# Optimization experiments

Measured on AMD Instinct MI355X. Metric: run time of the kernel, lower is better.

## Reference

```python
import jax, jax.numpy as jnp
import numpy as np

W_DIM = 72  # positional_encoding(3 coords, 12 freqs) -> 3*12*2
_F1 = np.array([1.0, 3.0, 3.0, 1.0], dtype=np.float32)
_F2 = np.outer(_F1, _F1); _F2 = _F2 / _F2.sum()  # normalized StyleGAN resample filter


def upsample2x(x):
    """Antialiased 2x upsample: zero-insertion + 4-tap [1,3,3,1] FIR, gain=4 (upfirdn2d)."""
    C = x.shape[1]
    k = jnp.tile(jnp.asarray(_F2 * 4.0, x.dtype)[None, None], (C, 1, 1, 1))  # [C,1,4,4]
    return jax.lax.conv_general_dilated(
        x, k, (1, 1), ((2, 2), (2, 2)), lhs_dilation=(2, 2),
        feature_group_count=C, dimension_numbers=('NCHW', 'OIHW', 'NCHW'))


def affine(w_vec, aw, ab):
    # FullyConnectedLayer: runtime weight gain 1/sqrt(w_dim), bias init 1
    return (w_vec @ aw.T) / np.sqrt(W_DIM) + ab


def mod_conv(x, weight, styles, demodulate=True, padding=1):
    """StyleGAN2 modulated conv2d (batch=1). weight [Co,Ci,k,k], styles [Ci]."""
    w = weight * styles[None, :, None, None]
    if demodulate:
        d = jax.lax.rsqrt(jnp.sum(w * w, axis=(1, 2, 3)) + 1e-8)
        w = w * d[:, None, None, None]
    return jax.lax.conv_general_dilated(
        x, w, (1, 1), ((padding, padding), (padding, padding)),
        dimension_numbers=('NCHW', 'OIHW', 'NCHW'))


def syn_layer(x, w_vec, aw, ab, cw, cb, up):
    s = affine(w_vec, aw, ab)
    if up:
        x = upsample2x(x)
    x = mod_conv(x, cw, s, True, 1)
    # bias_act: lrelu, gain sqrt(2), conv_clamp 256 (noise_strength init 0 -> no noise)
    x = jax.nn.leaky_relu(x + cb[None, :, None, None], 0.2) * np.sqrt(2.0)
    return jnp.clip(x, -256.0, 256.0)


def to_rgb(x, w_vec, aw, ab, cw, cb):
    s = affine(w_vec, aw, ab) / np.sqrt(cw.shape[1])  # ToRGB weight_gain 1/sqrt(Cin)
    y = mod_conv(x, cw, s, False, 0)
    return jnp.clip(y + cb[None, :, None, None], -256.0, 256.0)


def reference(rays, rgbs, conv_w, conv_b, bn_gamma, bn_beta, bn_mean, bn_var,
              a0_w, a0_b, w0, b0, a1_w, a1_b, w1, b1, t0_aw, t0_ab, t0_w, t0_b,
              a2_w, a2_b, w2, b2, a3_w, a3_b, w3, b3, t1_aw, t1_ab, t1_w, t1_b):
    # style vector from positional encoding of ray origin
    p = rays[0, :3, 0, 0]
    fb = 2.0 ** jnp.arange(12, dtype=rays.dtype)
    pts = (p[:, None] * fb[None, :]).reshape(-1)  # (36,)
    w_vec = jnp.concatenate([jnp.sin(pts), jnp.cos(pts)])  # (72,)
    # mapping: 1x1 conv + relu + BatchNorm2d (eval-mode)
    feat = jnp.einsum('oi,bihw->bohw', conv_w[:, :, 0, 0], rgbs) + conv_b[None, :, None, None]
    feat = jax.nn.relu(feat)
    inv = jax.lax.rsqrt(bn_var + 1e-5)
    feat = (feat - bn_mean[None, :, None, None]) * (inv * bn_gamma)[None, :, None, None] + bn_beta[None, :, None, None]
    rgb = feat[:, :3]
    # block0: 32ch@128 -> 256ch@256, skip-architecture ToRGB
    x = syn_layer(feat, w_vec, a0_w, a0_b, w0, b0, True)
    x = syn_layer(x, w_vec, a1_w, a1_b, w1, b1, False)
    img = upsample2x(rgb) + to_rgb(x, w_vec, t0_aw, t0_ab, t0_w, t0_b)
    # block1: 256ch@256 -> 128ch@512
    x = syn_layer(x, w_vec, a2_w, a2_b, w2, b2, True)
    x = syn_layer(x, w_vec, a3_w, a3_b, w3, b3, False)
    img = upsample2x(img) + to_rgb(x, w_vec, t1_aw, t1_ab, t1_w, t1_b)
    return img  # [1,3,512,512]


def setup_inputs() -> dict:
    key = jax.random.key(0)
    ks = jax.random.split(key, 16)
    rn = lambda k, s: jax.random.normal(k, s, dtype=jnp.float32)
    z = lambda s: jnp.zeros(s, jnp.float32)
    o = lambda s: jnp.ones(s, jnp.float32)
    inp = {}
    inp['rays'] = rn(ks[0], (1, 6, 128, 128))
    inp['rgbs'] = jax.random.uniform(ks[1], (1, 3, 128, 128), dtype=jnp.float32)
    inp['conv_w'] = rn(ks[2], (32, 3, 1, 1)); inp['conv_b'] = z((32,))
    inp['bn_gamma'] = o((32,)); inp['bn_beta'] = z((32,))
    inp['bn_mean'] = z((32,)); inp['bn_var'] = o((32,))
    inp['a0_w'] = rn(ks[3], (32, 72)); inp['a0_b'] = o((32,))
    inp['w0'] = rn(ks[4], (256, 32, 3, 3)); inp['b0'] = z((256,))
    inp['a1_w'] = rn(ks[5], (256, 72)); inp['a1_b'] = o((256,))
    inp['w1'] = rn(ks[6], (256, 256, 3, 3)); inp['b1'] = z((256,))
    inp['t0_aw'] = rn(ks[7], (256, 72)); inp['t0_ab'] = o((256,))
    inp['t0_w'] = rn(ks[8], (3, 256, 1, 1)); inp['t0_b'] = z((3,))
    inp['a2_w'] = rn(ks[9], (256, 72)); inp['a2_b'] = o((256,))
    inp['w2'] = rn(ks[10], (128, 256, 3, 3)); inp['b2'] = z((128,))
    inp['a3_w'] = rn(ks[11], (128, 72)); inp['a3_b'] = o((128,))
    inp['w3'] = rn(ks[12], (128, 128, 3, 3)); inp['b3'] = z((128,))
    inp['t1_aw'] = rn(ks[13], (128, 72)); inp['t1_ab'] = o((128,))
    inp['t1_w'] = rn(ks[14], (3, 128, 1, 1)); inp['t1_b'] = z((3,))
    return inp
```

## Files before the change

### kernel.cpp

```cpp
#include <hip/hip_runtime.h>
#include <cstddef>

typedef __attribute__((ext_vector_type(8))) short short8;
typedef __attribute__((ext_vector_type(4))) float f32x4;
typedef __attribute__((address_space(3))) void lds_void;
typedef const __attribute__((address_space(1))) void glob_void;

static const size_t OFF_S0    = 0;
static const size_t OFF_S1    = 64;
static const size_t OFF_S2    = 320;
static const size_t OFF_S3    = 576;
static const size_t OFF_MT0   = 704;
static const size_t OFF_MT1   = 1472;
static const size_t OFF_ZERO  = 1856;
static const size_t OFF_RGBF  = 2048;
static const size_t OFF_IMG0  = 51200;
static const size_t OFF_RGBP  = 247808;
static const size_t OFF_WQ0   = 1900544;
static const size_t OFF_WQ1   = 1937408;
static const size_t OFF_WQ2   = 2232320;
static const size_t OFF_WQ3   = 2379776;
static const size_t OFF_FEAT  = 2453504;
static const size_t OFF_UFEAT = 2715648;
static const size_t OFF_X1    = 4194304;
static const size_t OFF_X2    = 4194304;
static const size_t OFF_U     = 20971520;
static const size_t OFF_X0    = 20971520;

__device__ __forceinline__ unsigned short f2bf(float f) {
  unsigned int u = __float_as_uint(f);
  return (unsigned short)((u + 0x7FFFu + ((u >> 16) & 1u)) >> 16);
}
__device__ __forceinline__ float b2f(short h) {
  return __uint_as_float(((unsigned int)(unsigned short)h) << 16);
}

__global__ void __launch_bounds__(256) prep_kernel(
    const float* __restrict__ rays,
    const float* __restrict__ a0w, const float* __restrict__ a0b,
    const float* __restrict__ a1w, const float* __restrict__ a1b,
    const float* __restrict__ t0aw, const float* __restrict__ t0ab,
    const float* __restrict__ a2w, const float* __restrict__ a2b,
    const float* __restrict__ a3w, const float* __restrict__ a3b,
    const float* __restrict__ t1aw, const float* __restrict__ t1ab,
    const float* __restrict__ t0w, const float* __restrict__ t1w,
    float* __restrict__ ws)
{
  __shared__ float wv[72];
  __shared__ float st0l[256];
  __shared__ float st1l[128];
  const int tid = threadIdx.x;
  if (tid < 128) ws[OFF_ZERO + tid] = 0.f;
  if (tid < 36) {
    int i = tid / 12, j = tid % 12;
    float v = rays[i * 16384] * (float)(1 << j);
    wv[tid]      = sinf(v);
    wv[36 + tid] = cosf(v);
  }
  __syncthreads();
  const float inv72 = 0.11785113019775793f;

  if (tid < 32) {
    float d = 0.f;
    for (int k = 0; k < 72; ++k) d += wv[k] * a0w[tid * 72 + k];
    ws[OFF_S0 + tid] = fmaf(d, inv72, a0b[tid]);
  }
  {
    float d = 0.f;
    for (int k = 0; k < 72; ++k) d += wv[k] * a1w[tid * 72 + k];
    ws[OFF_S1 + tid] = fmaf(d, inv72, a1b[tid]);
  }
  {
    float d = 0.f;
    for (int k = 0; k < 72; ++k) d += wv[k] * t0aw[tid * 72 + k];
    st0l[tid] = fmaf(d, inv72, t0ab[tid]) * 0.0625f;
  }
  {
    float d = 0.f;
    for (int k = 0; k < 72; ++k) d += wv[k] * a2w[tid * 72 + k];
    ws[OFF_S2 + tid] = fmaf(d, inv72, a2b[tid]);
  }
  if (tid < 128) {
    float d = 0.f;
    for (int k = 0; k < 72; ++k) d += wv[k] * a3w[tid * 72 + k];
    ws[OFF_S3 + tid] = fmaf(d, inv72, a3b[tid]);
  }
  if (tid < 128) {
    float d = 0.f;
    for (int k = 0; k < 72; ++k) d += wv[k] * t1aw[tid * 72 + k];
    st1l[tid] = fmaf(d, inv72, t1ab[tid]) * 0.08838834764831845f;
  }
  __syncthreads();
  for (int i = tid; i < 768; i += 256) ws[OFF_MT0 + i] = t0w[i] * st0l[i & 255];
  for (int i = tid; i < 384; i += 256) ws[OFF_MT1 + i] = t1w[i] * st1l[i & 127];
}

__global__ void __launch_bounds__(256) modw_kernel(
    const float* __restrict__ w, const float* __restrict__ s,
    unsigned short* __restrict__ wq, int Ci, int Co)
{
  const int co = blockIdx.x;
  const int n = Ci * 9;
  float local = 0.f;
  for (int i = threadIdx.x; i < n; i += 256) {
    float v = w[co * n + i] * s[i / 9];
    local += v * v;
  }
#pragma unroll
  for (int off = 32; off >= 1; off >>= 1) local += __shfl_xor(local, off);
  __shared__ float red[4];
  if ((threadIdx.x & 63) == 0) red[threadIdx.x >> 6] = local;
  __syncthreads();
  const float d = rsqrtf(red[0] + red[1] + red[2] + red[3] + 1e-8f);
  for (int i = threadIdx.x; i < n; i += 256) {
    int ci = i / 9, t = i - ci * 9;
    wq[(((size_t)(ci >> 5) * 9 + t) * Co + co) * 32 + (ci & 31)] =
        f2bf(w[co * n + i] * s[ci] * d);
  }
}

__global__ void __launch_bounds__(256) feat_kernel(
    const float* __restrict__ rgbs, const float* __restrict__ cw, const float* __restrict__ cb,
    const float* __restrict__ gam, const float* __restrict__ bet,
    const float* __restrict__ mean, const float* __restrict__ var,
    unsigned short* __restrict__ feat, float* __restrict__ rgbf)
{
  const int p = blockIdx.x * 256 + threadIdx.x;
  const float r = rgbs[p], g = rgbs[16384 + p], b = rgbs[32768 + p];
  unsigned int pk[16];
#pragma unroll
  for (int co = 0; co < 32; ++co) {
    float v = cw[co * 3] * r + cw[co * 3 + 1] * g + cw[co * 3 + 2] * b + cb[co];
    v = fmaxf(v, 0.f);
    float inv = rsqrtf(var[co] + 1e-5f);
    v = (v - mean[co]) * (inv * gam[co]) + bet[co];
    if (co < 3) rgbf[co * 16384 + p] = v;
    unsigned int h = f2bf(v);
    if ((co & 1) == 0) pk[co >> 1] = h;
    else               pk[co >> 1] |= h << 16;
  }
  uint4* dst = reinterpret_cast<uint4*>(feat + (size_t)p * 32);
#pragma unroll
  for (int q = 0; q < 4; ++q)
    dst[q] = make_uint4(pk[q * 4], pk[q * 4 + 1], pk[q * 4 + 2], pk[q * 4 + 3]);
}

__global__ void __launch_bounds__(256) up2x_nhwc_kernel(
    const unsigned short* __restrict__ in, unsigned short* __restrict__ out,
    int H, int W, int c8s , int w2s )
{
  const int cid = blockIdx.x * 256 + threadIdx.x;
  const int k = cid & ((1 << c8s) - 1);
  const int pix = cid >> c8s;
  const int ey = pix >> w2s;
  const int ex = pix & ((1 << w2s) - 1);
  const int C = 8 << c8s;
  int ry0; float ay0, ay1;
  if (ey & 1) { ry0 = ey >> 1;       ay0 = 0.75f; ay1 = 0.25f; }
  else        { ry0 = (ey >> 1) - 1; ay0 = 0.25f; ay1 = 0.75f; }
  int cx0; float bx0, bx1;
  if (ex & 1) { cx0 = ex >> 1;       bx0 = 0.75f; bx1 = 0.25f; }
  else        { cx0 = (ex >> 1) - 1; bx0 = 0.25f; bx1 = 0.75f; }
  const short8 z = {0, 0, 0, 0, 0, 0, 0, 0};
  short8 v00 = z, v01 = z, v10 = z, v11 = z;
  const bool yo0 = (ry0 >= 0), yo1 = (ry0 + 1 < H);
  const bool xo0 = (cx0 >= 0), xo1 = (cx0 + 1 < W);
  if (yo0 && xo0) v00 = *reinterpret_cast<const short8*>(in + ((size_t)(ry0 * W + cx0) * C + k * 8));
  if (yo0 && xo1) v01 = *reinterpret_cast<const short8*>(in + ((size_t)(ry0 * W + cx0 + 1) * C + k * 8));
  if (yo1 && xo0) v10 = *reinterpret_cast<const short8*>(in + ((size_t)((ry0 + 1) * W + cx0) * C + k * 8));
  if (yo1 && xo1) v11 = *reinterpret_cast<const short8*>(in + ((size_t)((ry0 + 1) * W + cx0 + 1) * C + k * 8));
  unsigned int o[4];
#pragma unroll
  for (int j = 0; j < 8; ++j) {
    float f = ay0 * (bx0 * b2f(v00[j]) + bx1 * b2f(v01[j]))
            + ay1 * (bx0 * b2f(v10[j]) + bx1 * b2f(v11[j]));
    unsigned int h = f2bf(f);
    if ((j & 1) == 0) o[j >> 1] = h;
    else              o[j >> 1] |= h << 16;
  }
  *reinterpret_cast<uint4*>(out + (size_t)pix * C + k * 8) = make_uint4(o[0], o[1], o[2], o[3]);
}

template <bool FUSE_RGB>
__global__ void __launch_bounds__(512) conv3x3_mfma(
    const unsigned short* __restrict__ in,
    const unsigned short* __restrict__ wq,
    const float* __restrict__ bias,
    unsigned short* __restrict__ out,
    const float* __restrict__ rgbw,
    float* __restrict__ rgbp,
    const unsigned short* __restrict__ zpage,
    int H, int W, int Ci, int Co)
{
  const int tid  = threadIdx.x;
  const int lane = tid & 63;
  const int wv   = tid >> 6;
  const int wr   = wv & 3;
  const int wg   = wv >> 2;
  const int lo   = lane & 15, hi = lane >> 4;
  const int tpr  = W >> 4;
  const int T_y  = (blockIdx.x / tpr) << 4;
  const int T_x  = (blockIdx.x % tpr) << 4;
  const int cog  = (blockIdx.y * 2 + wg) << 6;

  __shared__ short8 xs[2][1296];
  __shared__ float  rw[FUSE_RGB ? 384 : 4];

  if (FUSE_RGB) {
    for (int i = tid; i < 3 * Co; i += 512) rw[i] = rgbw[i];
  }

  f32x4 acc[4][4];
#pragma unroll
  for (int a = 0; a < 4; ++a)
#pragma unroll
    for (int b = 0; b < 4; ++b) acc[a][b] = (f32x4){0.f, 0.f, 0.f, 0.f};

  const unsigned short* gsrc[3];
#pragma unroll
  for (int j = 0; j < 3; ++j) {
    const int s = j * 512 + tid;
    const int pix = s >> 2, kslot = s & 3;
    const int rr = pix / 18, cc = pix - rr * 18;
    const int gy = T_y - 1 + rr, gx = T_x - 1 + cc;
    const int k = kslot ^ ((cc >> 1) & 3);
    const bool inb = (s < 1296) && gy >= 0 && gy < H && gx >= 0 && gx < W;
    gsrc[j] = inb ? (in + ((size_t)(gy * W + gx) * Ci + (k << 3))) : zpage;
  }

#define STAGE(c, buf)                                                              \
  {                                                                                \
    const int cb_ = (c) << 5;                                                      \
    _Pragma("unroll")                                                              \
    for (int j = 0; j < 2; ++j)                                                    \
      __builtin_amdgcn_global_load_lds((glob_void*)(gsrc[j] + cb_),                \
                                       (lds_void*)&xs[buf][j * 512 + tid], 16, 0, 0); \
    if (tid < 272)                                                                 \
      __builtin_amdgcn_global_load_lds((glob_void*)(gsrc[2] + cb_),                \
                                       (lds_void*)&xs[buf][1024 + tid], 16, 0, 0); \
  }

  const int nch = Ci >> 5;
  const unsigned short* wa = wq + ((size_t)(cog + lo) << 5) + (hi << 3);
  const int wstride = Co << 5;
  short8 apf[2][4];

#define ALOAD(SLOT, STEP)                                                          \
  {                                                                                \
    const unsigned short* wp_ = wa + (size_t)(STEP) * wstride;                     \
    _Pragma("unroll")                                                              \
    for (int cf = 0; cf < 4; ++cf)                                                 \
      apf[SLOT][cf] = *reinterpret_cast<const short8*>(wp_ + (cf << 9));           \
  }

  STAGE(0, 0);
  __syncthreads();

  const int rstride = 18 << 2;
  for (int c = 0; c < nch; ++c) {
    const int cur = c & 1;
    if (c + 1 < nch) STAGE(c + 1, cur ^ 1);
    const int base = c * 9;
    ALOAD(0, base);

#pragma unroll
    for (int kx = 0; kx < 3; ++kx) {
      const int tx2  = lo + kx;
      const int xv_  = hi ^ ((tx2 >> 1) & 3);
      const int rowb = (((wr << 2) * 18 + tx2) << 2) + xv_;
      short8 b0 = xs[cur][rowb];
      short8 b1 = xs[cur][rowb + rstride];
      short8 b2 = xs[cur][rowb + 2 * rstride];
      short8 b3 = xs[cur][rowb + 3 * rstride];

      {
        constexpr int J0[3] = {0, 3, 6};
        const int j = J0[0] + 0; (void)j;
      }
      if (kx * 3 + 1 <= 8) ALOAD((kx * 3 + 1) & 1, base + ((kx * 3 + 1) % 3) * 3 + (kx * 3 + 1) / 3);
#pragma unroll
      for (int cf = 0; cf < 4; ++cf) {
        acc[cf][0] = __builtin_amdgcn_mfma_f32_16x16x32_bf16(apf[(kx * 3) & 1][cf], b0, acc[cf][0], 0, 0, 0);
        acc[cf][1] = __builtin_amdgcn_mfma_f32_16x16x32_bf16(apf[(kx * 3) & 1][cf], b1, acc[cf][1], 0, 0, 0);
        acc[cf][2] = __builtin_amdgcn_mfma_f32_16x16x32_bf16(apf[(kx * 3) & 1][cf], b2, acc[cf][2], 0, 0, 0);
        acc[cf][3] = __builtin_amdgcn_mfma_f32_16x16x32_bf16(apf[(kx * 3) & 1][cf], b3, acc[cf][3], 0, 0, 0);
      }
      b0 = xs[cur][rowb + 4 * rstride];
      if (kx * 3 + 2 <= 8) ALOAD((kx * 3 + 2) & 1, base + ((kx * 3 + 2) % 3) * 3 + (kx * 3 + 2) / 3);
#pragma unroll
      for (int cf = 0; cf < 4; ++cf) {
        acc[cf][0] = __builtin_amdgcn_mfma_f32_16x16x32_bf16(apf[(kx * 3 + 1) & 1][cf], b1, acc[cf][0], 0, 0, 0);
        acc[cf][1] = __builtin_amdgcn_mfma_f32_16x16x32_bf16(apf[(kx * 3 + 1) & 1][cf], b2, acc[cf][1], 0, 0, 0);
        acc[cf][2] = __builtin_amdgcn_mfma_f32_16x16x32_bf16(apf[(kx * 3 + 1) & 1][cf], b3, acc[cf][2], 0, 0, 0);
        acc[cf][3] = __builtin_amdgcn_mfma_f32_16x16x32_bf16(apf[(kx * 3 + 1) & 1][cf], b0, acc[cf][3], 0, 0, 0);
      }
      b1 = xs[cur][rowb + 5 * rstride];
      if (kx * 3 + 3 <= 8) ALOAD((kx * 3 + 3) & 1, base + ((kx * 3 + 3) % 3) * 3 + (kx * 3 + 3) / 3);
#pragma unroll
      for (int cf = 0; cf < 4; ++cf) {
        acc[cf][0] = __builtin_amdgcn_mfma_f32_16x16x32_bf16(apf[(kx * 3 + 2) & 1][cf], b2, acc[cf][0], 0, 0, 0);
        acc[cf][1] = __builtin_amdgcn_mfma_f32_16x16x32_bf16(apf[(kx * 3 + 2) & 1][cf], b3, acc[cf][1], 0, 0, 0);
        acc[cf][2] = __builtin_amdgcn_mfma_f32_16x16x32_bf16(apf[(kx * 3 + 2) & 1][cf], b0, acc[cf][2], 0, 0, 0);
        acc[cf][3] = __builtin_amdgcn_mfma_f32_16x16x32_bf16(apf[(kx * 3 + 2) & 1][cf], b1, acc[cf][3], 0, 0, 0);
      }
    }
    __syncthreads();
  }
#undef STAGE
#undef ALOAD

  const float rt2 = 1.41421356237309515f;
#pragma unroll
  for (int r = 0; r < 4; ++r) {
    const int gy = T_y + (wr << 2) + r;
    const int gx = T_x + lo;
    if (!FUSE_RGB) {
#pragma unroll
      for (int cf = 0; cf < 4; ++cf) {
        const int cb = cog + (cf << 4) + (hi << 2);
        const f32x4 bi = *reinterpret_cast<const f32x4*>(bias + cb);
        unsigned short h[4];
#pragma unroll
        for (int reg = 0; reg < 4; ++reg) {
          float vv = acc[cf][r][reg] + bi[reg];
          vv = (vv >= 0.f) ? vv : 0.2f * vv;
          vv *= rt2;
          vv = fminf(fmaxf(vv, -256.f), 256.f);
          h[reg] = f2bf(vv);
        }
        uint2 pk;
        pk.x = (unsigned int)h[0] | ((unsigned int)h[1] << 16);
        pk.y = (unsigned int)h[2] | ((unsigned int)h[3] << 16);
        *reinterpret_cast<uint2*>(out + (size_t)(gy * W + gx) * Co + cb) = pk;
      }
    } else {
      float p0 = 0.f, p1 = 0.f, p2 = 0.f;
#pragma unroll
      for (int cf = 0; cf < 4; ++cf) {
        const int cb = cog + (cf << 4) + (hi << 2);
        const f32x4 bi = *reinterpret_cast<const f32x4*>(bias + cb);
#pragma unroll
        for (int reg = 0; reg < 4; ++reg) {
          float vv = acc[cf][r][reg] + bi[reg];
          vv = (vv >= 0.f) ? vv : 0.2f * vv;
          vv *= rt2;
          vv = fminf(fmaxf(vv, -256.f), 256.f);
          p0 = fmaf(rw[cb + reg], vv, p0);
          p1 = fmaf(rw[Co + cb + reg], vv, p1);
          p2 = fmaf(rw[2 * Co + cb + reg], vv, p2);
        }
      }
      p0 += __shfl_xor(p0, 16); p0 += __shfl_xor(p0, 32);
      p1 += __shfl_xor(p1, 16); p1 += __shfl_xor(p1, 32);
      p2 += __shfl_xor(p2, 16); p2 += __shfl_xor(p2, 32);
      if (hi == 0) {
        const size_t HWs = (size_t)H * W;
        const size_t px  = (size_t)gy * W + gx;
        rgbp[((size_t)wg * 3 + 0) * HWs + px] = p0;
        rgbp[((size_t)wg * 3 + 1) * HWs + px] = p1;
        rgbp[((size_t)wg * 3 + 2) * HWs + px] = p2;
      }
    }
  }
}

__device__ __forceinline__ float up2x_sample(const float* __restrict__ im, int H, int W,
                                             int oy, int ox)
{
  int my = oy >> 1, mx = ox >> 1;
  int ry0; float ay0, ay1;
  if (oy & 1) { ry0 = my;     ay0 = 0.75f; ay1 = 0.25f; }
  else        { ry0 = my - 1; ay0 = 0.25f; ay1 = 0.75f; }
  int cx0; float bx0, bx1;
  if (ox & 1) { cx0 = mx;     bx0 = 0.75f; bx1 = 0.25f; }
  else        { cx0 = mx - 1; bx0 = 0.25f; bx1 = 0.75f; }
  float v00 = (ry0 >= 0    && cx0 >= 0   ) ? im[ry0 * W + cx0]           : 0.f;
  float v01 = (ry0 >= 0    && cx0 + 1 < W) ? im[ry0 * W + cx0 + 1]       : 0.f;
  float v10 = (ry0 + 1 < H && cx0 >= 0   ) ? im[(ry0 + 1) * W + cx0]     : 0.f;
  float v11 = (ry0 + 1 < H && cx0 + 1 < W) ? im[(ry0 + 1) * W + cx0 + 1] : 0.f;
  return ay0 * (bx0 * v00 + bx1 * v01) + ay1 * (bx0 * v10 + bx1 * v11);
}

__global__ void __launch_bounds__(256) img0_kernel(
    const float* __restrict__ rgbf, const unsigned short* __restrict__ x1,
    const float* __restrict__ mt0g, const float* __restrict__ tb,
    float* __restrict__ img0)
{
  __shared__ float mt[768];
  const int tid = threadIdx.x;
  for (int i = tid; i < 768; i += 256) mt[i] = mt0g[i];
  __syncthreads();
  const int p = blockIdx.x * 256 + tid;
  const unsigned short* xp = x1 + (size_t)p * 256;
  float a0 = 0.f, a1 = 0.f, a2 = 0.f;
  for (int i8 = 0; i8 < 32; ++i8) {
    const short8 v = *reinterpret_cast<const short8*>(xp + i8 * 8);
#pragma unroll
    for (int j = 0; j < 8; ++j) {
      const float xv = b2f(v[j]);
      const int ci = i8 * 8 + j;
      a0 = fmaf(mt[ci],       xv, a0);
      a1 = fmaf(mt[256 + ci], xv, a1);
      a2 = fmaf(mt[512 + ci], xv, a2);
    }
  }
  const int oy = p >> 8, ox = p & 255;
  float av[3] = {a0, a1, a2};
#pragma unroll
  for (int o = 0; o < 3; ++o) {
    float y = fminf(fmaxf(av[o] + tb[o], -256.f), 256.f);
    img0[o * 65536 + p] = up2x_sample(rgbf + o * 16384, 128, 128, oy, ox) + y;
  }
}

__global__ void __launch_bounds__(256) final_kernel(
    const float* __restrict__ img0, const float* __restrict__ rgbp,
    const float* __restrict__ tb, float* __restrict__ out)
{
  const int p = blockIdx.x * 256 + threadIdx.x;
  const int oy = p >> 9, ox = p & 511;
#pragma unroll
  for (int o = 0; o < 3; ++o) {
    float a = rgbp[(0 * 3 + o) * 262144 + p] + rgbp[(1 * 3 + o) * 262144 + p];
    float y = fminf(fmaxf(a + tb[o], -256.f), 256.f);
    out[o * 262144 + p] = up2x_sample(img0 + o * 65536, 256, 256, oy, ox) + y;
  }
}

extern "C" void kernel_launch(void* const* d_in, const int* in_sizes, int n_in,
                              void* d_out, int out_size, void* d_ws, size_t ws_size,
                              hipStream_t stream)
{
  const float* rays   = (const float*)d_in[0];
  const float* rgbs   = (const float*)d_in[1];
  const float* conv_w = (const float*)d_in[2];
  const float* conv_b = (const float*)d_in[3];
  const float* bn_g   = (const float*)d_in[4];
  const float* bn_b   = (const float*)d_in[5];
  const float* bn_m   = (const float*)d_in[6];
  const float* bn_v   = (const float*)d_in[7];
  const float* a0_w   = (const float*)d_in[8];
  const float* a0_b   = (const float*)d_in[9];
  const float* w0     = (const float*)d_in[10];
  const float* b0     = (const float*)d_in[11];
  const float* a1_w   = (const float*)d_in[12];
  const float* a1_b   = (const float*)d_in[13];
  const float* w1     = (const float*)d_in[14];
  const float* b1     = (const float*)d_in[15];
  const float* t0_aw  = (const float*)d_in[16];
  const float* t0_ab  = (const float*)d_in[17];
  const float* t0_w   = (const float*)d_in[18];
  const float* t0_b   = (const float*)d_in[19];
  const float* a2_w   = (const float*)d_in[20];
  const float* a2_b   = (const float*)d_in[21];
  const float* w2     = (const float*)d_in[22];
  const float* b2     = (const float*)d_in[23];
  const float* a3_w   = (const float*)d_in[24];
  const float* a3_b   = (const float*)d_in[25];
  const float* w3     = (const float*)d_in[26];
  const float* b3     = (const float*)d_in[27];
  const float* t1_aw  = (const float*)d_in[28];
  const float* t1_ab  = (const float*)d_in[29];
  const float* t1_w   = (const float*)d_in[30];
  const float* t1_b   = (const float*)d_in[31];

  float* ws  = (float*)d_ws;
  float* out = (float*)d_out;

  unsigned short* wq0   = (unsigned short*)(ws + OFF_WQ0);
  unsigned short* wq1   = (unsigned short*)(ws + OFF_WQ1);
  unsigned short* wq2   = (unsigned short*)(ws + OFF_WQ2);
  unsigned short* wq3   = (unsigned short*)(ws + OFF_WQ3);
  unsigned short* featb = (unsigned short*)(ws + OFF_FEAT);
  unsigned short* ufeat = (unsigned short*)(ws + OFF_UFEAT);
  unsigned short* x0b   = (unsigned short*)(ws + OFF_X0);
  unsigned short* x1b   = (unsigned short*)(ws + OFF_X1);
  unsigned short* x2b   = (unsigned short*)(ws + OFF_X2);
  unsigned short* Ub    = (unsigned short*)(ws + OFF_U);
  const unsigned short* zpage = (const unsigned short*)(ws + OFF_ZERO);

  prep_kernel<<<1, 256, 0, stream>>>(rays, a0_w, a0_b, a1_w, a1_b, t0_aw, t0_ab,
                                     a2_w, a2_b, a3_w, a3_b, t1_aw, t1_ab,
                                     t0_w, t1_w, ws);
  modw_kernel<<<256, 256, 0, stream>>>(w0, ws + OFF_S0, wq0, 32, 256);
  modw_kernel<<<256, 256, 0, stream>>>(w1, ws + OFF_S1, wq1, 256, 256);
  modw_kernel<<<128, 256, 0, stream>>>(w2, ws + OFF_S2, wq2, 256, 128);
  modw_kernel<<<128, 256, 0, stream>>>(w3, ws + OFF_S3, wq3, 128, 128);
  feat_kernel<<<64, 256, 0, stream>>>(rgbs, conv_w, conv_b, bn_g, bn_b, bn_m, bn_v,
                                      featb, ws + OFF_RGBF);
  up2x_nhwc_kernel<<<1024, 256, 0, stream>>>(featb, ufeat, 128, 128, 2, 8);
  conv3x3_mfma<false><<<dim3(256, 2), 512, 0, stream>>>(
      ufeat, wq0, b0, x0b, nullptr, nullptr, zpage, 256, 256, 32, 256);
  conv3x3_mfma<false><<<dim3(256, 2), 512, 0, stream>>>(
      x0b, wq1, b1, x1b, nullptr, nullptr, zpage, 256, 256, 256, 256);
  img0_kernel<<<256, 256, 0, stream>>>(ws + OFF_RGBF, x1b, ws + OFF_MT0, t0_b,
                                       ws + OFF_IMG0);
  up2x_nhwc_kernel<<<32768, 256, 0, stream>>>(x1b, Ub, 256, 256, 5, 9);
  conv3x3_mfma<false><<<dim3(1024, 1), 512, 0, stream>>>(
      Ub, wq2, b2, x2b, nullptr, nullptr, zpage, 512, 512, 256, 128);
  conv3x3_mfma<true><<<dim3(1024, 1), 512, 0, stream>>>(
      x2b, wq3, b3, nullptr, ws + OFF_MT1, ws + OFF_RGBP, zpage, 512, 512, 128, 128);
  final_kernel<<<1024, 256, 0, stream>>>(ws + OFF_IMG0, ws + OFF_RGBP, t1_b, out);
}
```

Measured before the change: 467.5 us.

## Stage modulated conv weights through double-buffered swizzled LDS instead of direct global loads

Weights for the implicit-GEMM conv are now copied into a double-buffered LDS tile with async global_load_lds, one kx column (3 ky taps) at a time, instead of each wave reading its A fragments straight from global memory. The weight packing kernel applies an XOR swizzle on the 8-element slot, keyed by output channel, so the LDS fragment reads avoid bank conflicts. This lets the two wave groups of a block share one weight fetch and hides global latency. The cost is a __syncthreads per kx step (three per channel chunk instead of one) and about 48 KB of extra LDS, which may reduce occupancy.

```diff
diff --git a/kernel.cpp b/kernel.cpp
--- a/kernel.cpp
+++ b/kernel.cpp
@@ -112,9 +112,12 @@
   if ((threadIdx.x & 63) == 0) red[threadIdx.x >> 6] = local;
   __syncthreads();
   const float d = rsqrtf(red[0] + red[1] + red[2] + red[3] + 1e-8f);
+  const int sxor = (co & 3) ^ ((co >> 2) & 3);
   for (int i = threadIdx.x; i < n; i += 256) {
     int ci = i / 9, t = i - ci * 9;
-    wq[(((size_t)(ci >> 5) * 9 + t) * Co + co) * 32 + (ci & 31)] =
+    int kk = ci & 31;
+    int sl = (kk >> 3) ^ sxor;
+    wq[(((size_t)(ci >> 5) * 9 + t) * Co + co) * 32 + (sl << 3) + (kk & 7)] =
         f2bf(w[co * n + i] * s[ci] * d);
   }
 }
@@ -201,9 +204,11 @@
   const int tpr  = W >> 4;
   const int T_y  = (blockIdx.x / tpr) << 4;
   const int T_x  = (blockIdx.x % tpr) << 4;
-  const int cog  = (blockIdx.y * 2 + wg) << 6;
+  const int cogB = blockIdx.y << 7;
+  const int cog  = cogB + (wg << 6);
 
   __shared__ short8 xs[2][1296];
+  __shared__ short8 wlds[2][1536];
   __shared__ float  rw[FUSE_RGB ? 384 : 4];
 
   if (FUSE_RGB) {
@@ -240,32 +245,42 @@
                                        (lds_void*)&xs[buf][1024 + tid], 16, 0, 0); \
   }
 
-  const int nch = Ci >> 5;
-  const unsigned short* wa = wq + ((size_t)(cog + lo) << 5) + (hi << 3);
-  const int wstride = Co << 5;
-  short8 apf[2][4];
-
-#define ALOAD(SLOT, STEP)                                                          \
+#define STAGE_W(C, KX, BUF)                                                        \
   {                                                                                \
-    const unsigned short* wp_ = wa + (size_t)(STEP) * wstride;                     \
+    _Pragma("unroll")                                                              \
+    for (int j = 0; j < 3; ++j) {                                                  \
+      const unsigned short* src_ =                                                 \
+          wq + ((size_t)((C) * 9 + j * 3 + (KX)) * Co + cogB) * 32 + tid * 8;      \
+      __builtin_amdgcn_global_load_lds((glob_void*)src_,                           \
+                                       (lds_void*)&wlds[BUF][(j << 9) + tid], 16, 0, 0); \
+    }                                                                              \
+  }
+
+  const int sxa   = (lo & 3) ^ ((lo >> 2) & 3);
+  const int wbase = (((wg << 6) + lo) << 2) + (hi ^ sxa);
+#define ALOADW(SLOT, KY, BUF)                                                      \
+  {                                                                                \
     _Pragma("unroll")                                                              \
     for (int cf = 0; cf < 4; ++cf)                                                 \
-      apf[SLOT][cf] = *reinterpret_cast<const short8*>(wp_ + (cf << 9));           \
+      apf[SLOT][cf] = wlds[BUF][((KY) << 9) + wbase + (cf << 6)];                  \
   }
 
   STAGE(0, 0);
+  STAGE_W(0, 0, 0);
   __syncthreads();
 
-  const int rstride = 18 << 2;
+  const int nch = Ci >> 5;
+  const int rstride = 72;
+  int wb = 0;
   for (int c = 0; c < nch; ++c) {
     const int cur = c & 1;
-    if (c + 1 < nch) STAGE(c + 1, cur ^ 1);
-    const int base = c * 9;
-    ALOAD(0, base);
-
-#pragma unroll
-    for (int kx = 0; kx < 3; ++kx) {
-      const int tx2  = lo + kx;
+#pragma unroll
+    for (int g = 0; g < 3; ++g) {
+      if (g < 2)             { STAGE_W(c, g + 1, wb ^ 1); }
+      else if (c + 1 < nch)  { STAGE_W(c + 1, 0, wb ^ 1); }
+      if (g == 0 && c + 1 < nch) STAGE(c + 1, cur ^ 1);
+
+      const int tx2  = lo + g;
       const int xv_  = hi ^ ((tx2 >> 1) & 3);
       const int rowb = (((wr << 2) * 18 + tx2) << 2) + xv_;
       short8 b0 = xs[cur][rowb];
@@ -273,41 +288,40 @@
       short8 b2 = xs[cur][rowb + 2 * rstride];
       short8 b3 = xs[cur][rowb + 3 * rstride];
 
-      {
-        constexpr int J0[3] = {0, 3, 6};
-        const int j = J0[0] + 0; (void)j;
-      }
-      if (kx * 3 + 1 <= 8) ALOAD((kx * 3 + 1) & 1, base + ((kx * 3 + 1) % 3) * 3 + (kx * 3 + 1) / 3);
+      short8 apf[2][4];
+      ALOADW(0, 0, wb);
+      ALOADW(1, 1, wb);
 #pragma unroll
       for (int cf = 0; cf < 4; ++cf) {
-        acc[cf][0] = __builtin_amdgcn_mfma_f32_16x16x32_bf16(apf[(kx * 3) & 1][cf], b0, acc[cf][0], 0, 0, 0);
-        acc[cf][1] = __builtin_amdgcn_mfma_f32_16x16x32_bf16(apf[(kx * 3) & 1][cf], b1, acc[cf][1], 0, 0, 0);
-        acc[cf][2] = __builtin_amdgcn_mfma_f32_16x16x32_bf16(apf[(kx * 3) & 1][cf], b2, acc[cf][2], 0, 0, 0);
-        acc[cf][3] = __builtin_amdgcn_mfma_f32_16x16x32_bf16(apf[(kx * 3) & 1][cf], b3, acc[cf][3], 0, 0, 0);
+        acc[cf][0] = __builtin_amdgcn_mfma_f32_16x16x32_bf16(apf[0][cf], b0, acc[cf][0], 0, 0, 0);
+        acc[cf][1] = __builtin_amdgcn_mfma_f32_16x16x32_bf16(apf[0][cf], b1, acc[cf][1], 0, 0, 0);
+        acc[cf][2] = __builtin_amdgcn_mfma_f32_16x16x32_bf16(apf[0][cf], b2, acc[cf][2], 0, 0, 0);
+        acc[cf][3] = __builtin_amdgcn_mfma_f32_16x16x32_bf16(apf[0][cf], b3, acc[cf][3], 0, 0, 0);
       }
       b0 = xs[cur][rowb + 4 * rstride];
-      if (kx * 3 + 2 <= 8) ALOAD((kx * 3 + 2) & 1, base + ((kx * 3 + 2) % 3) * 3 + (kx * 3 + 2) / 3);
+      ALOADW(0, 2, wb);
 #pragma unroll
       for (int cf = 0; cf < 4; ++cf) {
-        acc[cf][0] = __builtin_amdgcn_mfma_f32_16x16x32_bf16(apf[(kx * 3 + 1) & 1][cf], b1, acc[cf][0], 0, 0, 0);
-        acc[cf][1] = __builtin_amdgcn_mfma_f32_16x16x32_bf16(apf[(kx * 3 + 1) & 1][cf], b2, acc[cf][1], 0, 0, 0);
-        acc[cf][2] = __builtin_amdgcn_mfma_f32_16x16x32_bf16(apf[(kx * 3 + 1) & 1][cf], b3, acc[cf][2], 0, 0, 0);
-        acc[cf][3] = __builtin_amdgcn_mfma_f32_16x16x32_bf16(apf[(kx * 3 + 1) & 1][cf], b0, acc[cf][3], 0, 0, 0);
+        acc[cf][0] = __builtin_amdgcn_mfma_f32_16x16x32_bf16(apf[1][cf], b1, acc[cf][0], 0, 0, 0);
+        acc[cf][1] = __builtin_amdgcn_mfma_f32_16x16x32_bf16(apf[1][cf], b2, acc[cf][1], 0, 0, 0);
+        acc[cf][2] = __builtin_amdgcn_mfma_f32_16x16x32_bf16(apf[1][cf], b3, acc[cf][2], 0, 0, 0);
+        acc[cf][3] = __builtin_amdgcn_mfma_f32_16x16x32_bf16(apf[1][cf], b0, acc[cf][3], 0, 0, 0);
       }
       b1 = xs[cur][rowb + 5 * rstride];
-      if (kx * 3 + 3 <= 8) ALOAD((kx * 3 + 3) & 1, base + ((kx * 3 + 3) % 3) * 3 + (kx * 3 + 3) / 3);
 #pragma unroll
       for (int cf = 0; cf < 4; ++cf) {
-        acc[cf][0] = __builtin_amdgcn_mfma_f32_16x16x32_bf16(apf[(kx * 3 + 2) & 1][cf], b2, acc[cf][0], 0, 0, 0);
-        acc[cf][1] = __builtin_amdgcn_mfma_f32_16x16x32_bf16(apf[(kx * 3 + 2) & 1][cf], b3, acc[cf][1], 0, 0, 0);
-        acc[cf][2] = __builtin_amdgcn_mfma_f32_16x16x32_bf16(apf[(kx * 3 + 2) & 1][cf], b0, acc[cf][2], 0, 0, 0);
-        acc[cf][3] = __builtin_amdgcn_mfma_f32_16x16x32_bf16(apf[(kx * 3 + 2) & 1][cf], b1, acc[cf][3], 0, 0, 0);
+        acc[cf][0] = __builtin_amdgcn_mfma_f32_16x16x32_bf16(apf[0][cf], b2, acc[cf][0], 0, 0, 0);
+        acc[cf][1] = __builtin_amdgcn_mfma_f32_16x16x32_bf16(apf[0][cf], b3, acc[cf][1], 0, 0, 0);
+        acc[cf][2] = __builtin_amdgcn_mfma_f32_16x16x32_bf16(apf[0][cf], b0, acc[cf][2], 0, 0, 0);
+        acc[cf][3] = __builtin_amdgcn_mfma_f32_16x16x32_bf16(apf[0][cf], b1, acc[cf][3], 0, 0, 0);
       }
+      __syncthreads();
+      wb ^= 1;
     }
-    __syncthreads();
   }
 #undef STAGE
-#undef ALOAD
+#undef STAGE_W
+#undef ALOADW
 
   const float rt2 = 1.41421356237309515f;
 #pragma unroll
```

Measured after the change: 463.4 us. Within noise of the previous version (-0.9%).
